# Kernel tuning notes

Hardware: AMD Instinct MI355X
Metric: run time of the kernel (lower is better)

The kernel has to match this reference:

```python
import jax, jax.numpy as jnp
import numpy as np

VOCAB, EMB, HID, OUT = 128, 128, 256, 2
B, T = 128, 2048


def setup_inputs() -> dict:
    key = jax.random.key(0)
    ks = jax.random.split(key, 8)
    s_ih = 1.0 / np.sqrt(HID)
    inp = {
        "x": jax.random.randint(ks[0], (B, T), 0, VOCAB, dtype=jnp.int32),
        "emb": jax.random.normal(ks[1], (VOCAB, EMB), jnp.float32),
        "W_ih": jax.random.uniform(ks[2], (4 * HID, EMB), jnp.float32, -s_ih, s_ih),
        "W_hh": jax.random.uniform(ks[3], (4 * HID, HID), jnp.float32, -s_ih, s_ih),
        "b_ih": jax.random.uniform(ks[4], (4 * HID,), jnp.float32, -s_ih, s_ih),
        "b_hh": jax.random.uniform(ks[5], (4 * HID,), jnp.float32, -s_ih, s_ih),
        "fc_W": jax.random.normal(ks[6], (OUT, HID), jnp.float32) * np.sqrt(6.0 / (HID + OUT)),
        "fc_b": jnp.zeros((OUT,), jnp.float32),
    }
    return inp


def _lstm_last_hidden(xe, W_ih, W_hh, b_ih, b_hh):
    # xe: [B, T, E]. Precompute all input-to-hidden gate projections (batched GEMM).
    Bsz = xe.shape[0]
    H = W_hh.shape[1]
    xg = jnp.einsum('bte,ge->tbg', xe, W_ih) + (b_ih + b_hh)  # [T, B, 4H]

    def step(carry, xt):
        h, c = carry
        g = xt + h @ W_hh.T                 # [B, 4H]
        i, f, gg, o = jnp.split(g, 4, axis=-1)  # PyTorch gate order i,f,g,o
        i = jax.nn.sigmoid(i)
        f = jax.nn.sigmoid(f)
        gg = jnp.tanh(gg)
        o = jax.nn.sigmoid(o)
        c = f * c + i * gg
        h = o * jnp.tanh(c)
        return (h, c), None

    h0 = jnp.zeros((Bsz, H), xe.dtype)
    c0 = jnp.zeros((Bsz, H), xe.dtype)
    (hT, _), _ = jax.lax.scan(step, (h0, c0), xg)
    return hT  # == output[:, -1, :] for a uni-directional LSTM


def reference(x, emb, W_ih, W_hh, b_ih, b_hh, fc_W, fc_b):
    xe = emb[x]                                   # [B, T, E] embedding lookup
    hT = _lstm_last_hidden(xe, W_ih, W_hh, b_ih, b_hh)
    logits = hT @ fc_W.T + fc_b                   # [B, OUT]
    return logits
```

## Files before the change

kernel.cpp:

```cpp
#include <hip/hip_runtime.h>

#define T_LEN 2048
#define HID   256
#define G4    1024
#define EMBD  128
#define VOCAB 128
#define OUTC  2
#define BSUB  4
#define NCHAIN 32
#define CHK   64
#define XCHS  72
#define HSB   288
#define LOG2E 1.44269504088896340736f

typedef int   i32x4 __attribute__((ext_vector_type(4)));
typedef float f32x4 __attribute__((ext_vector_type(4)));

__device__ __align__(16) float Pbuf[VOCAB * G4];
__device__ __align__(16) signed char Wqb[G4 * HID];
__device__ float Winv[G4];

__global__ void build_P(const float* __restrict__ emb, const float* __restrict__ W_ih,
                        const float* __restrict__ b_ih, const float* __restrict__ b_hh) {
    const int v = blockIdx.x >> 2;
    const int c = ((blockIdx.x & 3) << 8) + threadIdx.x;
    __shared__ float es[EMBD];
    if (threadIdx.x < EMBD) es[threadIdx.x] = emb[v * EMBD + threadIdx.x];
    __syncthreads();
    const float* wr = W_ih + c * EMBD;
    float acc = 0.f;
    #pragma unroll 8
    for (int e = 0; e < EMBD; ++e) acc += es[e] * wr[e];
    const float ks = ((c >> 8) == 2) ? (-2.f * LOG2E) : (-LOG2E);
    const int g  = c >> 8;
    const int rr = c & 255;
    const int wi = rr >> 5;
    const int nt = (rr >> 4) & 1;
    const int l  = rr & 15;
    Pbuf[v * G4 + wi * 128 + l * 8 + nt * 4 + g] = (acc + b_ih[c] + b_hh[c]) * ks;
}

__global__ void quant_W(const float* __restrict__ W_hh) {
    const int row = blockIdx.x;
    const int k   = threadIdx.x;
    __shared__ float red[4];
    const float wv = W_hh[row * HID + k];
    float a = fabsf(wv);
    #pragma unroll
    for (int o = 32; o > 0; o >>= 1) a = fmaxf(a, __shfl_down(a, o, 64));
    if ((k & 63) == 0) red[k >> 6] = a;
    __syncthreads();
    const float m = fmaxf(fmaxf(fmaxf(red[0], red[1]), red[2]), fmaxf(red[3], 1e-30f));
    Wqb[row * HID + k] = (signed char)(int)rintf(wv * (127.f / m));
    const float ks = ((row >> 8) == 2) ? (-2.f * LOG2E) : (-LOG2E);
    if (k == 0) Winv[row] = m * (1.f / (127.f * 127.f)) * ks;
}

__device__ __forceinline__ float sig_p(float p) {
    return __builtin_amdgcn_rcpf(1.f + __builtin_amdgcn_exp2f(p));
}

__global__ __launch_bounds__(512, 2) void lstm_chain(
        const int* __restrict__ x, const float* __restrict__ fc_W,
        const float* __restrict__ fc_b, float* __restrict__ out) {
    __shared__ __align__(16) signed char habuf[2][BSUB * HSB];
    __shared__ int   xch[BSUB * XCHS];
    __shared__ float hfin[BSUB * HID];

    const int tid  = threadIdx.x;
    const int w    = tid >> 6;
    const int lane = tid & 63;
    const int l15  = lane & 15;
    const int quad = lane >> 4;
    const int bbase = blockIdx.x * BSUB;
    const int ub    = w * 32;

    i32x4 Bf[2][4][4];
    float winvv[2][4];
    #pragma unroll
    for (int nt = 0; nt < 2; ++nt) {
        #pragma unroll
        for (int g = 0; g < 4; ++g) {
            const int row = g * HID + ub + nt * 16 + l15;
            const signed char* wr = Wqb + (size_t)row * HID;
            winvv[nt][g] = Winv[row];
            #pragma unroll
            for (int kt = 0; kt < 4; ++kt)
                Bf[nt][g][kt] = *(const i32x4*)(wr + kt * 64 + quad * 16);
        }
    }

    if (tid < BSUB * HSB / 4) ((int*)habuf[0])[tid] = 0;

    float cst[2] = {0.f, 0.f};
    f32x4 xga0, xga1, xgb0, xgb1;
    const i32x4 zero4 = {0, 0, 0, 0};
    const float* pbase = Pbuf + w * 128 + l15 * 8;
    const signed char* habA = habuf[0] + (l15 >> 2) * HSB + quad * 16;
    const signed char* habB = habuf[1] + (l15 >> 2) * HSB + quad * 16;

#define GATHER(TT, X0, X1)                                                    \
    {                                                                         \
        const int xv = xch[quad * XCHS + (TT)];                               \
        const f32x4* pb = (const f32x4*)(pbase + (size_t)xv * G4);            \
        X0 = pb[0];                                                           \
        X1 = pb[1];                                                           \
    }

#define GATE(NT, ACC, XG, HN, TCUR)                                           \
    {                                                                         \
        const int col = ub + NT * 16 + l15;                                   \
        const float pi = fmaf((float)ACC[0][0], winvv[NT][0], XG[0]);         \
        const float pf = fmaf((float)ACC[1][0], winvv[NT][1], XG[1]);         \
        const float pg = fmaf((float)ACC[2][0], winvv[NT][2], XG[2]);         \
        const float po = fmaf((float)ACC[3][0], winvv[NT][3], XG[3]);         \
        const float is = sig_p(pi);                                           \
        const float fs = sig_p(pf);                                           \
        const float gt = fmaf(2.f, sig_p(pg), -1.f);                          \
        const float os = sig_p(po);                                           \
        const float c  = fmaf(fs, cst[NT], is * gt);                          \
        cst[NT] = c;                                                          \
        const float hq = fmaf(254.f, sig_p(c * (-2.f * LOG2E)), -127.f) * os; \
        (HN)[quad * HSB + col] = (signed char)(int)rintf(hq);                 \
        if ((TCUR) == T_LEN - 1) hfin[quad * HID + col] = hq * (1.f / 127.f); \
    }

#define STEP(HAB, HN, XC0, XC1, XN0, XN1, PF, TT, TCUR)                       \
    {                                                                         \
        i32x4 af[4];                                                          \
        _Pragma("unroll")                                                     \
        for (int kt = 0; kt < 4; ++kt)                                        \
            af[kt] = *(const i32x4*)((HAB) + kt * 64);                        \
        if (PF) GATHER((TT), XN0, XN1);                                       \
        i32x4 a0[4], a1[4];                                                   \
        _Pragma("unroll")                                                     \
        for (int g = 0; g < 4; ++g)                                           \
            a0[g] = __builtin_amdgcn_mfma_i32_16x16x64_i8(af[0], Bf[0][g][0], zero4, 0, 0, 0); \
        _Pragma("unroll")                                                     \
        for (int kt = 1; kt < 4; ++kt)                                        \
            _Pragma("unroll")                                                 \
            for (int g = 0; g < 4; ++g)                                       \
                a0[g] = __builtin_amdgcn_mfma_i32_16x16x64_i8(af[kt], Bf[0][g][kt], a0[g], 0, 0, 0); \
        _Pragma("unroll")                                                     \
        for (int g = 0; g < 4; ++g)                                           \
            a1[g] = __builtin_amdgcn_mfma_i32_16x16x64_i8(af[0], Bf[1][g][0], zero4, 0, 0, 0); \
        _Pragma("unroll")                                                     \
        for (int kt = 1; kt < 4; ++kt)                                        \
            _Pragma("unroll")                                                 \
            for (int g = 0; g < 4; ++g)                                       \
                a1[g] = __builtin_amdgcn_mfma_i32_16x16x64_i8(af[kt], Bf[1][g][kt], a1[g], 0, 0, 0); \
          \
        GATE(0, a0, XC0, HN, TCUR);                                           \
        GATE(1, a1, XC1, HN, TCUR);                                           \
        __syncthreads();                                                      \
    }

    #pragma unroll 1
    for (int ch = 0; ch < T_LEN / CHK; ++ch) {
        if (tid < BSUB * CHK)
            xch[(tid >> 6) * XCHS + (tid & 63)] =
                x[(bbase + (tid >> 6)) * T_LEN + ch * CHK + (tid & 63)];
        __syncthreads();
        GATHER(0, xga0, xga1);
        const int tb = ch * CHK;
        #pragma unroll 1
        for (int tt = 0; tt < CHK; tt += 2) {
            STEP(habA, habuf[1], xga0, xga1, xgb0, xgb1, 1, tt + 1, tb + tt);
            STEP(habB, habuf[0], xgb0, xgb1, xga0, xga1, (tt < CHK - 2), tt + 2, tb + tt + 1);
        }
    }
#undef STEP
#undef GATE
#undef GATHER

    if (tid < BSUB * OUTC) {
        const int b = tid >> 1, o = tid & 1;
        float s = fc_b[o];
        #pragma unroll 8
        for (int j = 0; j < HID; ++j) s += hfin[b * HID + j] * fc_W[o * HID + j];
        out[(bbase + b) * OUTC + o] = s;
    }
}

extern "C" void kernel_launch(void* const* d_in, const int* in_sizes, int n_in,
                              void* d_out, int out_size, void* d_ws, size_t ws_size,
                              hipStream_t stream) {
    const int*   x    = (const int*)  d_in[0];
    const float* emb  = (const float*)d_in[1];
    const float* W_ih = (const float*)d_in[2];
    const float* W_hh = (const float*)d_in[3];
    const float* b_ih = (const float*)d_in[4];
    const float* b_hh = (const float*)d_in[5];
    const float* fc_W = (const float*)d_in[6];
    const float* fc_b = (const float*)d_in[7];
    float* out = (float*)d_out;
    (void)d_ws; (void)ws_size;

    build_P<<<dim3(VOCAB * 4), dim3(256), 0, stream>>>(emb, W_ih, b_ih, b_hh);
    quant_W<<<dim3(G4), dim3(HID), 0, stream>>>(W_hh);
    lstm_chain<<<dim3(NCHAIN), dim3(512), 0, stream>>>(x, fc_W, fc_b, out);
}
```

Measured before the change: 1.663 ms.

## Halve batch per workgroup and spread gate epilogue across quads

Each workgroup now handles 2 batch rows instead of 4, and 64 workgroups are launched instead of 32. The gate nonlinearity work per lane drops from two columns to one, because quads now split across batch and column tile. The Pbuf layout is reordered to match. The aim is to shorten the serial per-step critical path (transcendentals plus the barrier) and use more CUs. The cost is that half the MFMA rows now do redundant work, and twice as many workgroups each load the full weight set.

```diff
diff --git a/kernel.cpp b/kernel.cpp
--- a/kernel.cpp
+++ b/kernel.cpp
@@ -6,8 +6,8 @@
 #define EMBD  128
 #define VOCAB 128
 #define OUTC  2
-#define BSUB  4
-#define NCHAIN 32
+#define BSUB  2
+#define NWG   64
 #define CHK   64
 #define XCHS  72
 #define HSB   288
@@ -37,7 +37,7 @@
     const int wi = rr >> 5;
     const int nt = (rr >> 4) & 1;
     const int l  = rr & 15;
-    Pbuf[v * G4 + wi * 128 + l * 8 + nt * 4 + g] = (acc + b_ih[c] + b_hh[c]) * ks;
+    Pbuf[v * G4 + wi * 128 + nt * 64 + l * 4 + g] = (acc + b_ih[c] + b_hh[c]) * ks;
 }
 
 __global__ void quant_W(const float* __restrict__ W_hh) {
@@ -74,64 +74,46 @@
     const int quad = lane >> 4;
     const int bbase = blockIdx.x * BSUB;
     const int ub    = w * 32;
+    const int bq    = quad >> 1;
+    const int ntq   = quad & 1;
+    const int colq  = ub + ntq * 16 + l15;
 
     i32x4 Bf[2][4][4];
-    float winvv[2][4];
     #pragma unroll
-    for (int nt = 0; nt < 2; ++nt) {
+    for (int nt = 0; nt < 2; ++nt)
         #pragma unroll
         for (int g = 0; g < 4; ++g) {
-            const int row = g * HID + ub + nt * 16 + l15;
-            const signed char* wr = Wqb + (size_t)row * HID;
-            winvv[nt][g] = Winv[row];
+            const signed char* wr = Wqb + (size_t)(g * HID + ub + nt * 16 + l15) * HID;
             #pragma unroll
             for (int kt = 0; kt < 4; ++kt)
                 Bf[nt][g][kt] = *(const i32x4*)(wr + kt * 64 + quad * 16);
         }
-    }
+    float winvv[4];
+    #pragma unroll
+    for (int g = 0; g < 4; ++g) winvv[g] = Winv[g * HID + colq];
 
     if (tid < BSUB * HSB / 4) ((int*)habuf[0])[tid] = 0;
 
-    float cst[2] = {0.f, 0.f};
-    f32x4 xga0, xga1, xgb0, xgb1;
+    float cst = 0.f;
+    f32x4 xga, xgb;
     const i32x4 zero4 = {0, 0, 0, 0};
-    const float* pbase = Pbuf + w * 128 + l15 * 8;
-    const signed char* habA = habuf[0] + (l15 >> 2) * HSB + quad * 16;
-    const signed char* habB = habuf[1] + (l15 >> 2) * HSB + quad * 16;
+    const float* pbase = Pbuf + w * 128 + ntq * 64 + l15 * 4;
+    const signed char* habA = habuf[0] + (l15 >> 3) * HSB + quad * 16;
+    const signed char* habB = habuf[1] + (l15 >> 3) * HSB + quad * 16;
 
-#define GATHER(TT, X0, X1)                                                    \
+#define GATHER(TT, XG)                                                        \
     {                                                                         \
-        const int xv = xch[quad * XCHS + (TT)];                               \
-        const f32x4* pb = (const f32x4*)(pbase + (size_t)xv * G4);            \
-        X0 = pb[0];                                                           \
-        X1 = pb[1];                                                           \
+        const int xv = xch[bq * XCHS + (TT)];                                 \
+        XG = *(const f32x4*)(pbase + (size_t)xv * G4);                        \
     }
 
-#define GATE(NT, ACC, XG, HN, TCUR)                                           \
-    {                                                                         \
-        const int col = ub + NT * 16 + l15;                                   \
-        const float pi = fmaf((float)ACC[0][0], winvv[NT][0], XG[0]);         \
-        const float pf = fmaf((float)ACC[1][0], winvv[NT][1], XG[1]);         \
-        const float pg = fmaf((float)ACC[2][0], winvv[NT][2], XG[2]);         \
-        const float po = fmaf((float)ACC[3][0], winvv[NT][3], XG[3]);         \
-        const float is = sig_p(pi);                                           \
-        const float fs = sig_p(pf);                                           \
-        const float gt = fmaf(2.f, sig_p(pg), -1.f);                          \
-        const float os = sig_p(po);                                           \
-        const float c  = fmaf(fs, cst[NT], is * gt);                          \
-        cst[NT] = c;                                                          \
-        const float hq = fmaf(254.f, sig_p(c * (-2.f * LOG2E)), -127.f) * os; \
-        (HN)[quad * HSB + col] = (signed char)(int)rintf(hq);                 \
-        if ((TCUR) == T_LEN - 1) hfin[quad * HID + col] = hq * (1.f / 127.f); \
-    }
-
-#define STEP(HAB, HN, XC0, XC1, XN0, XN1, PF, TT, TCUR)                       \
+#define STEP(HAB, HN, XC, XN, PF, TT, TCUR)                                   \
     {                                                                         \
         i32x4 af[4];                                                          \
         _Pragma("unroll")                                                     \
         for (int kt = 0; kt < 4; ++kt)                                        \
             af[kt] = *(const i32x4*)((HAB) + kt * 64);                        \
-        if (PF) GATHER((TT), XN0, XN1);                                       \
+        if (PF) GATHER((TT), XN);                                             \
         i32x4 a0[4], a1[4];                                                   \
         _Pragma("unroll")                                                     \
         for (int g = 0; g < 4; ++g)                                           \
@@ -149,9 +131,20 @@
             _Pragma("unroll")                                                 \
             for (int g = 0; g < 4; ++g)                                       \
                 a1[g] = __builtin_amdgcn_mfma_i32_16x16x64_i8(af[kt], Bf[1][g][kt], a1[g], 0, 0, 0); \
-          \
-        GATE(0, a0, XC0, HN, TCUR);                                           \
-        GATE(1, a1, XC1, HN, TCUR);                                           \
+                         \
+        const int gi_ = ntq ? a1[0][0] : a0[0][0];                            \
+        const int gf_ = ntq ? a1[1][0] : a0[1][0];                            \
+        const int gg_ = ntq ? a1[2][0] : a0[2][0];                            \
+        const int go_ = ntq ? a1[3][0] : a0[3][0];                            \
+        const float is = sig_p(fmaf((float)gi_, winvv[0], XC[0]));            \
+        const float fs = sig_p(fmaf((float)gf_, winvv[1], XC[1]));            \
+        const float gt = fmaf(2.f, sig_p(fmaf((float)gg_, winvv[2], XC[2])), -1.f); \
+        const float os = sig_p(fmaf((float)go_, winvv[3], XC[3]));            \
+        const float c  = fmaf(fs, cst, is * gt);                              \
+        cst = c;                                                              \
+        const float hq = fmaf(254.f, sig_p(c * (-2.f * LOG2E)), -127.f) * os; \
+        (HN)[bq * HSB + colq] = (signed char)(int)rintf(hq);                  \
+        if ((TCUR) == T_LEN - 1) hfin[bq * HID + colq] = hq * (1.f / 127.f);  \
         __syncthreads();                                                      \
     }
 
@@ -161,16 +154,15 @@
             xch[(tid >> 6) * XCHS + (tid & 63)] =
                 x[(bbase + (tid >> 6)) * T_LEN + ch * CHK + (tid & 63)];
         __syncthreads();
-        GATHER(0, xga0, xga1);
+        GATHER(0, xga);
         const int tb = ch * CHK;
         #pragma unroll 1
         for (int tt = 0; tt < CHK; tt += 2) {
-            STEP(habA, habuf[1], xga0, xga1, xgb0, xgb1, 1, tt + 1, tb + tt);
-            STEP(habB, habuf[0], xgb0, xgb1, xga0, xga1, (tt < CHK - 2), tt + 2, tb + tt + 1);
+            STEP(habA, habuf[1], xga, xgb, 1, tt + 1, tb + tt);
+            STEP(habB, habuf[0], xgb, xga, (tt < CHK - 2), tt + 2, tb + tt + 1);
         }
     }
 #undef STEP
-#undef GATE
 #undef GATHER
 
     if (tid < BSUB * OUTC) {
@@ -198,5 +190,5 @@
 
     build_P<<<dim3(VOCAB * 4), dim3(256), 0, stream>>>(emb, W_ih, b_ih, b_hh);
     quant_W<<<dim3(G4), dim3(HID), 0, stream>>>(W_hh);
-    lstm_chain<<<dim3(NCHAIN), dim3(512), 0, stream>>>(x, fc_W, fc_b, out);
+    lstm_chain<<<dim3(NWG), dim3(512), 0, stream>>>(x, fc_W, fc_b, out);
 }
```

Result: faster. 1.412 ms, median of 2 (-15.1%).
